# Kernel optimization log

Measured on AMD Instinct MI355X. Metric: run time of the kernel, lower is better.

Reference implementation:

```python
import jax, jax.numpy as jnp
import numpy as np

N = 100000        # nodes
E = 1_600_000     # edges (avg degree 16)
IN = 128          # in_feats
HID = 64          # hidden_feats
H = 3             # num_heads
OUT = 16          # out_feats
NEG_SLOPE = 0.2   # DGL GATConv default LeakyReLU slope


def setup_inputs() -> dict:
    key = jax.random.key(0)
    ks = jax.random.split(key, 16)
    f = lambda k, shape, s=0.1: (jax.random.normal(k, shape, jnp.float32) * s)
    return {
        "features": f(ks[0], (N, IN), 1.0),
        "src": jax.random.randint(ks[1], (E,), 0, N),
        "dst": jax.random.randint(ks[2], (E,), 0, N),
        # GATConv 1: in -> (H, HID)
        "W1": f(ks[3], (IN, H * HID)),
        "al1": f(ks[4], (H, HID)),
        "ar1": f(ks[5], (H, HID)),
        "b1": f(ks[6], (H, HID)),
        # GATConv 2: H*HID -> (H, HID)
        "W2": f(ks[7], (H * HID, H * HID)),
        "al2": f(ks[8], (H, HID)),
        "ar2": f(ks[9], (H, HID)),
        "b2": f(ks[10], (H, HID)),
        # MLP head
        "w3": f(ks[11], (H * HID, HID)),
        "b3": f(ks[12], (HID,)),
        "w4": f(ks[13], (HID, OUT)),
        "b4": f(ks[14], (OUT,)),
    }


def gat_layer(x, src, dst, W, al, ar, b):
    # feat: (N, H, D) projected features
    feat = (x @ W).reshape(-1, H, HID)
    el = jnp.einsum('nhd,hd->nh', feat, al)   # (N, H)
    er = jnp.einsum('nhd,hd->nh', feat, ar)   # (N, H)
    e = el[src] + er[dst]                     # (E, H) edge scores
    e = jnp.where(e > 0, e, NEG_SLOPE * e)    # LeakyReLU
    # numerically stable softmax over incoming edges of each dst node
    m = jax.lax.stop_gradient(jax.ops.segment_max(e, dst, num_segments=N))
    ex = jnp.exp(e - m[dst])
    s = jax.ops.segment_sum(ex, dst, num_segments=N)
    alpha = ex / s[dst]                       # (E, H)
    # message passing: scatter alpha-weighted src features to dst
    out = jax.ops.segment_sum(alpha[:, :, None] * feat[src], dst, num_segments=N)
    return jax.nn.relu(out + b)               # (N, H, D)


def reference(features, src, dst, W1, al1, ar1, b1, W2, al2, ar2, b2, w3, b3, w4, b4):
    x = gat_layer(features, src, dst, W1, al1, ar1, b1).reshape(N, H * HID)
    x = gat_layer(x, src, dst, W2, al2, ar2, b2).reshape(N, H * HID)
    h = jax.nn.relu(x @ w3 + b3)
    return h @ w4 + b4
```

## Files before the change

kernel.cpp:

```cpp
#include <hip/hip_runtime.h>
#include <cstdint>
#include <cstddef>

#define NN   100000
#define EE   1600000
#define INF_ 128
#define HIDF 64
#define NH   3
#define FEAT 192
#define OUTF 16
#define NEG  0.2f

#define NI4  25000
#define NB   98

typedef unsigned short ushort_t;
typedef unsigned int   uint_t;

__device__ __forceinline__ float bf2f(ushort_t u) {
    return __uint_as_float(((uint_t)u) << 16);
}
__device__ __forceinline__ ushort_t f2bf(float f) {
    uint_t b = __float_as_uint(f);
    return (ushort_t)((b + 0x7FFFu + ((b >> 16) & 1u)) >> 16);
}


__global__ void hist_kernel(const int* __restrict__ dst, int* __restrict__ counts) {
    int e = blockIdx.x * 256 + threadIdx.x;
    if (e < EE) atomicAdd(&counts[dst[e]], 1);
}

__global__ __launch_bounds__(256) void blocksum_kernel(const int* __restrict__ counts,
                                                       int* __restrict__ bsum) {
    int t = threadIdx.x;
    int idx4 = blockIdx.x * 256 + t;
    int s = 0;
    if (idx4 < NI4) {
        int4 v = ((const int4*)counts)[idx4];
        s = v.x + v.y + v.z + v.w;
    }
    __shared__ int sd[4];
    for (int o = 32; o; o >>= 1) s += __shfl_down(s, o, 64);
    if ((t & 63) == 0) sd[t >> 6] = s;
    __syncthreads();
    if (t == 0) bsum[blockIdx.x] = sd[0] + sd[1] + sd[2] + sd[3];
}

__global__ __launch_bounds__(128) void scanb_kernel(int* __restrict__ bsum) {
    __shared__ int sd[128];
    int t = threadIdx.x;
    int v = (t < NB) ? bsum[t] : 0;
    sd[t] = v;
    __syncthreads();
    for (int o = 1; o < 128; o <<= 1) {
        int u = (t >= o) ? sd[t - o] : 0;
        __syncthreads();
        sd[t] += u;
        __syncthreads();
    }
    if (t < NB) bsum[t] = sd[t] - v;
}

__global__ __launch_bounds__(256) void scanfinal_kernel(const int* __restrict__ counts,
                                                        const int* __restrict__ bsum,
                                                        int* __restrict__ row_ptr,
                                                        int* __restrict__ cursor) {
    __shared__ int sd[256];
    int t = threadIdx.x;
    int idx4 = blockIdx.x * 256 + t;
    int4 v = make_int4(0, 0, 0, 0);
    if (idx4 < NI4) v = ((const int4*)counts)[idx4];
    int s = v.x + v.y + v.z + v.w;
    sd[t] = s;
    __syncthreads();
    for (int o = 1; o < 256; o <<= 1) {
        int u = (t >= o) ? sd[t - o] : 0;
        __syncthreads();
        sd[t] += u;
        __syncthreads();
    }
    int base = bsum[blockIdx.x] + sd[t] - s;
    if (idx4 < NI4) {
        int4 r;
        r.x = base;
        r.y = base + v.x;
        r.z = base + v.x + v.y;
        r.w = base + v.x + v.y + v.z;
        ((int4*)row_ptr)[idx4] = r;
        ((int4*)cursor)[idx4]  = r;
    }
    if (blockIdx.x == 0 && t == 0) row_ptr[NN] = EE;
}

__global__ void scatter_kernel(const int* __restrict__ src, const int* __restrict__ dst,
                               int* __restrict__ cursor, int* __restrict__ ssrc,
                               int* __restrict__ sdst) {
    int e = blockIdx.x * 256 + threadIdx.x;
    if (e < EE) {
        int d = dst[e];
        int p = atomicAdd(&cursor[d], 1);
        ssrc[p] = src[e];
        sdst[p] = d;
    }
}


__global__ __launch_bounds__(256) void edgew_kernel(const int* __restrict__ ssrc,
                                                    const int* __restrict__ sdst,
                                                    const float* __restrict__ el,
                                                    const float* __restrict__ er,
                                                    float* __restrict__ wgt) {
    int p = blockIdx.x * 256 + threadIdx.x;
    if (p >= EE) return;
    int s = ssrc[p], d = sdst[p];
    float a0 = el[s * 3 + 0] + er[d * 3 + 0]; a0 = a0 > 0.f ? a0 : NEG * a0;
    float a1 = el[s * 3 + 1] + er[d * 3 + 1]; a1 = a1 > 0.f ? a1 : NEG * a1;
    float a2 = el[s * 3 + 2] + er[d * 3 + 2]; a2 = a2 > 0.f ? a2 : NEG * a2;
    wgt[p * 3 + 0] = __expf(a0);
    wgt[p * 3 + 1] = __expf(a1);
    wgt[p * 3 + 2] = __expf(a2);
}


template <int K, int N, bool BIAS, bool RELU, bool ELER, bool A_BF16, bool C_BF16>
__global__ __launch_bounds__(256) void gemm64_kernel(const void* __restrict__ Av,
                                                     const float* __restrict__ B,
                                                     const float* __restrict__ bias,
                                                     void* __restrict__ Cv,
                                                     const float* __restrict__ al,
                                                     const float* __restrict__ ar,
                                                     float* __restrict__ el,
                                                     float* __restrict__ er) {
    __shared__ float As[32][64];
    __shared__ float Bs[32][64];
    const int m0 = blockIdx.x * 64;
    const int n0 = blockIdx.y * 64;
    const int t  = threadIdx.x;
    const int tr = t >> 4;
    const int tc = t & 15;

    float acc[4][4] = {};

    for (int kt = 0; kt < K; kt += 32) {
        if (A_BF16) {
            const ushort_t* A = (const ushort_t*)Av;
            int row = t >> 2, c8 = (t & 3) * 8;
            int gr = m0 + row;
            if (gr < NN) {
                uint4 v = *(const uint4*)(A + (size_t)gr * K + kt + c8);
                As[c8 + 0][row] = bf2f((ushort_t)(v.x & 0xffff));
                As[c8 + 1][row] = bf2f((ushort_t)(v.x >> 16));
                As[c8 + 2][row] = bf2f((ushort_t)(v.y & 0xffff));
                As[c8 + 3][row] = bf2f((ushort_t)(v.y >> 16));
                As[c8 + 4][row] = bf2f((ushort_t)(v.z & 0xffff));
                As[c8 + 5][row] = bf2f((ushort_t)(v.z >> 16));
                As[c8 + 6][row] = bf2f((ushort_t)(v.w & 0xffff));
                As[c8 + 7][row] = bf2f((ushort_t)(v.w >> 16));
            } else {
#pragma unroll
                for (int j = 0; j < 8; ++j) As[c8 + j][row] = 0.f;
            }
        } else {
            const float* A = (const float*)Av;
            int f = t;
#pragma unroll
            for (int it = 0; it < 2; ++it, f += 256) {
                int row = f >> 3, c4 = (f & 7) * 4;
                float4 v = make_float4(0.f, 0.f, 0.f, 0.f);
                int gr = m0 + row;
                if (gr < NN) v = *(const float4*)(A + (size_t)gr * K + kt + c4);
                As[c4 + 0][row] = v.x;
                As[c4 + 1][row] = v.y;
                As[c4 + 2][row] = v.z;
                As[c4 + 3][row] = v.w;
            }
        }
        {
            int f = t;
#pragma unroll
            for (int it = 0; it < 2; ++it, f += 256) {
                int row = f >> 4, c4 = (f & 15) * 4;
                *(float4*)&Bs[row][c4] = *(const float4*)(B + (size_t)(kt + row) * N + n0 + c4);
            }
        }
        __syncthreads();
#pragma unroll
        for (int k = 0; k < 32; ++k) {
            float4 a = *(const float4*)&As[k][tr * 4];
            float4 b = *(const float4*)&Bs[k][tc * 4];
            acc[0][0] += a.x * b.x; acc[0][1] += a.x * b.y; acc[0][2] += a.x * b.z; acc[0][3] += a.x * b.w;
            acc[1][0] += a.y * b.x; acc[1][1] += a.y * b.y; acc[1][2] += a.y * b.z; acc[1][3] += a.y * b.w;
            acc[2][0] += a.z * b.x; acc[2][1] += a.z * b.y; acc[2][2] += a.z * b.z; acc[2][3] += a.z * b.w;
            acc[3][0] += a.w * b.x; acc[3][1] += a.w * b.y; acc[3][2] += a.w * b.z; acc[3][3] += a.w * b.w;
        }
        __syncthreads();
    }

    float4 bv = make_float4(0.f, 0.f, 0.f, 0.f);
    if (BIAS) bv = *(const float4*)(bias + n0 + tc * 4);
#pragma unroll
    for (int i = 0; i < 4; ++i) {
        int row = m0 + tr * 4 + i;
        if (row >= NN) continue;
        float4 r;
        r.x = acc[i][0]; r.y = acc[i][1]; r.z = acc[i][2]; r.w = acc[i][3];
        if (BIAS) { r.x += bv.x; r.y += bv.y; r.z += bv.z; r.w += bv.w; }
        if (RELU) {
            r.x = fmaxf(r.x, 0.f); r.y = fmaxf(r.y, 0.f);
            r.z = fmaxf(r.z, 0.f); r.w = fmaxf(r.w, 0.f);
        }
        if (C_BF16) {
            ushort4 u;
            u.x = f2bf(r.x); u.y = f2bf(r.y); u.z = f2bf(r.z); u.w = f2bf(r.w);
            *(ushort4*)((ushort_t*)Cv + (size_t)row * N + n0 + tc * 4) = u;
        } else {
            *(float4*)((float*)Cv + (size_t)row * N + n0 + tc * 4) = r;
        }
    }

    if (ELER) {
        const int h = blockIdx.y;
        float4 va = *(const float4*)(al + h * HIDF + tc * 4);
        float4 vb = *(const float4*)(ar + h * HIDF + tc * 4);
#pragma unroll
        for (int i = 0; i < 4; ++i) {
            float pl = acc[i][0] * va.x + acc[i][1] * va.y + acc[i][2] * va.z + acc[i][3] * va.w;
            float pr = acc[i][0] * vb.x + acc[i][1] * vb.y + acc[i][2] * vb.z + acc[i][3] * vb.w;
#pragma unroll
            for (int o = 1; o < 16; o <<= 1) {
                pl += __shfl_xor(pl, o, 16);
                pr += __shfl_xor(pr, o, 16);
            }
            int row = m0 + tr * 4 + i;
            if (tc == 0 && row < NN) {
                el[row * NH + h] = pl;
                er[row * NH + h] = pr;
            }
        }
    }
}


template <int K, int M, int ROWS, bool BIAS, bool RELU>
__global__ void rowgemm_kernel(const float* __restrict__ A, const float* __restrict__ W,
                               const float* __restrict__ bias, float* __restrict__ C) {
    __shared__ float a[ROWS][K];
    const int BT = M * ROWS;
    int r0 = blockIdx.x * ROWS;
    for (int i = threadIdx.x; i < ROWS * K; i += BT) {
        int rr = i / K, kk = i - rr * K;
        int row = r0 + rr;
        a[rr][kk] = (row < NN) ? A[(size_t)row * K + kk] : 0.f;
    }
    __syncthreads();
    int rr = threadIdx.x / M, c = threadIdx.x - rr * M;
    int row = r0 + rr;
    if (row >= NN) return;
    float acc = 0.f;
#pragma unroll
    for (int k = 0; k < K; ++k) acc += a[rr][k] * W[k * M + c];
    if (BIAS) acc += bias[c];
    if (RELU) acc = fmaxf(acc, 0.f);
    C[(size_t)row * M + c] = acc;
}


__global__ __launch_bounds__(256) void aggregate_kernel(
    const int* __restrict__ row_ptr, const int* __restrict__ ssrc,
    const float* __restrict__ wgt,
    const ushort_t* __restrict__ featb, const float* __restrict__ bias,
    ushort_t* __restrict__ outb) {
    int w = blockIdx.x * 4 + (threadIdx.x >> 6);
    if (w >= NN) return;
    int lane = threadIdx.x & 63;
    int beg = row_ptr[w], end = row_ptr[w + 1];

    float s0 = 0.f, s1 = 0.f, s2 = 0.f;
    float acc0 = 0.f, acc1 = 0.f, acc2 = 0.f;
    for (int p = beg; p < end; ++p) {
        int s = __builtin_amdgcn_readfirstlane(ssrc[p]);
        float w0 = wgt[p * 3 + 0];
        float w1 = wgt[p * 3 + 1];
        float w2 = wgt[p * 3 + 2];
        s0 += w0; s1 += w1; s2 += w2;
        const ushort_t* fr = featb + (size_t)s * FEAT;
        acc0 += w0 * bf2f(fr[lane]);
        acc1 += w1 * bf2f(fr[64 + lane]);
        acc2 += w2 * bf2f(fr[128 + lane]);
    }

    float r0, r1, r2;
    if (end > beg) { r0 = acc0 / s0; r1 = acc1 / s1; r2 = acc2 / s2; }
    else           { r0 = r1 = r2 = 0.f; }
    r0 += bias[lane]; r1 += bias[64 + lane]; r2 += bias[128 + lane];
    outb[(size_t)w * FEAT + lane]       = f2bf(fmaxf(r0, 0.f));
    outb[(size_t)w * FEAT + 64 + lane]  = f2bf(fmaxf(r1, 0.f));
    outb[(size_t)w * FEAT + 128 + lane] = f2bf(fmaxf(r2, 0.f));
}


extern "C" void kernel_launch(void* const* d_in, const int* in_sizes, int n_in,
                              void* d_out, int out_size, void* d_ws, size_t ws_size,
                              hipStream_t stream) {
    const float* features = (const float*)d_in[0];
    const int*   src      = (const int*)d_in[1];
    const int*   dst      = (const int*)d_in[2];
    const float* W1  = (const float*)d_in[3];
    const float* al1 = (const float*)d_in[4];
    const float* ar1 = (const float*)d_in[5];
    const float* b1  = (const float*)d_in[6];
    const float* W2  = (const float*)d_in[7];
    const float* al2 = (const float*)d_in[8];
    const float* ar2 = (const float*)d_in[9];
    const float* b2  = (const float*)d_in[10];
    const float* w3  = (const float*)d_in[11];
    const float* b3  = (const float*)d_in[12];
    const float* w4  = (const float*)d_in[13];
    const float* b4  = (const float*)d_in[14];
    float* out = (float*)d_out;

    char* p = (char*)d_ws;
    ushort_t* featb = (ushort_t*)p; p += (size_t)NN * FEAT * 2;
    ushort_t* xb    = (ushort_t*)p; p += (size_t)NN * FEAT * 2;
    float* scratch  = (float*)p;    p += (size_t)NN * HIDF * 4;
    float* el  = (float*)p; p += (size_t)NN * NH * 4;
    float* er  = (float*)p; p += (size_t)NN * NH * 4;
    int* counts  = (int*)p;  p += (size_t)NN * 4;
    int* row_ptr = (int*)p;  p += (size_t)(NN + 4) * 4;
    int* cursor  = (int*)p;  p += (size_t)NN * 4;
    int* ssrc    = (int*)p;  p += (size_t)EE * 4;
    int* sdst    = (int*)p;  p += (size_t)EE * 4;
    int* bsum    = (int*)p;  p += 128 * 4;

    float* wgt = scratch;
    float* hid = scratch;

    const int GM = (NN + 63) / 64;
    const int GE = (EE + 255) / 256;

    hipMemsetAsync(counts, 0, (size_t)NN * 4, stream);
    hist_kernel<<<GE, 256, 0, stream>>>(dst, counts);
    blocksum_kernel<<<NB, 256, 0, stream>>>(counts, bsum);
    scanb_kernel<<<1, 128, 0, stream>>>(bsum);
    scanfinal_kernel<<<NB, 256, 0, stream>>>(counts, bsum, row_ptr, cursor);
    scatter_kernel<<<GE, 256, 0, stream>>>(src, dst, cursor, ssrc, sdst);

    gemm64_kernel<INF_, FEAT, false, false, true, false, true>
        <<<dim3(GM, FEAT / 64), 256, 0, stream>>>(features, W1, nullptr, featb, al1, ar1, el, er);
    edgew_kernel<<<GE, 256, 0, stream>>>(ssrc, sdst, el, er, wgt);
    aggregate_kernel<<<(NN + 3) / 4, 256, 0, stream>>>(row_ptr, ssrc, wgt, featb, b1, xb);

    gemm64_kernel<FEAT, FEAT, false, false, true, true, true>
        <<<dim3(GM, FEAT / 64), 256, 0, stream>>>(xb, W2, nullptr, featb, al2, ar2, el, er);
    edgew_kernel<<<GE, 256, 0, stream>>>(ssrc, sdst, el, er, wgt);
    aggregate_kernel<<<(NN + 3) / 4, 256, 0, stream>>>(row_ptr, ssrc, wgt, featb, b2, xb);

    gemm64_kernel<FEAT, HIDF, true, true, false, true, false>
        <<<dim3(GM, 1), 256, 0, stream>>>(xb, w3, b3, hid, nullptr, nullptr, nullptr, nullptr);
    rowgemm_kernel<HIDF, OUTF, 16, true, false><<<NN / 16, 256, 0, stream>>>(hid, w4, b4, out);
}
```

Before: 889.5 us.

## Load edge indices and weights cooperatively per wavefront and broadcast via shuffles

Edge softmax weights are stored as three separate per-head arrays instead of interleaved triples. The aggregation kernel now loads up to 64 edge source indices and weights at once with coalesced per-lane loads. It reduces the denominators with a butterfly shuffle and broadcasts each edge's index and weights via shuffles in the inner loop. This replaces serialized per-edge uniform loads, whose latency sits on the critical path of the gather, at the cost of extra shuffle instructions per edge.

```diff
diff --git a/kernel.cpp b/kernel.cpp
--- a/kernel.cpp
+++ b/kernel.cpp
@@ -110,16 +110,18 @@
                                                     const int* __restrict__ sdst,
                                                     const float* __restrict__ el,
                                                     const float* __restrict__ er,
-                                                    float* __restrict__ wgt) {
+                                                    float* __restrict__ wgt0,
+                                                    float* __restrict__ wgt1,
+                                                    float* __restrict__ wgt2) {
     int p = blockIdx.x * 256 + threadIdx.x;
     if (p >= EE) return;
     int s = ssrc[p], d = sdst[p];
     float a0 = el[s * 3 + 0] + er[d * 3 + 0]; a0 = a0 > 0.f ? a0 : NEG * a0;
     float a1 = el[s * 3 + 1] + er[d * 3 + 1]; a1 = a1 > 0.f ? a1 : NEG * a1;
     float a2 = el[s * 3 + 2] + er[d * 3 + 2]; a2 = a2 > 0.f ? a2 : NEG * a2;
-    wgt[p * 3 + 0] = __expf(a0);
-    wgt[p * 3 + 1] = __expf(a1);
-    wgt[p * 3 + 2] = __expf(a2);
+    wgt0[p] = __expf(a0);
+    wgt1[p] = __expf(a1);
+    wgt2[p] = __expf(a2);
 }
 
 
@@ -268,7 +270,8 @@
 
 __global__ __launch_bounds__(256) void aggregate_kernel(
     const int* __restrict__ row_ptr, const int* __restrict__ ssrc,
-    const float* __restrict__ wgt,
+    const float* __restrict__ wgt0, const float* __restrict__ wgt1,
+    const float* __restrict__ wgt2,
     const ushort_t* __restrict__ featb, const float* __restrict__ bias,
     ushort_t* __restrict__ outb) {
     int w = blockIdx.x * 4 + (threadIdx.x >> 6);
@@ -278,16 +281,36 @@
 
     float s0 = 0.f, s1 = 0.f, s2 = 0.f;
     float acc0 = 0.f, acc1 = 0.f, acc2 = 0.f;
-    for (int p = beg; p < end; ++p) {
-        int s = __builtin_amdgcn_readfirstlane(ssrc[p]);
-        float w0 = wgt[p * 3 + 0];
-        float w1 = wgt[p * 3 + 1];
-        float w2 = wgt[p * 3 + 2];
-        s0 += w0; s1 += w1; s2 += w2;
-        const ushort_t* fr = featb + (size_t)s * FEAT;
-        acc0 += w0 * bf2f(fr[lane]);
-        acc1 += w1 * bf2f(fr[64 + lane]);
-        acc2 += w2 * bf2f(fr[128 + lane]);
+
+    for (int c = beg; c < end; c += 64) {
+        int n = min(64, end - c);
+        int   sv  = 0;
+        float wv0 = 0.f, wv1 = 0.f, wv2 = 0.f;
+        if (lane < n) {
+            sv  = ssrc[c + lane];
+            wv0 = wgt0[c + lane];
+            wv1 = wgt1[c + lane];
+            wv2 = wgt2[c + lane];
+        }
+        float t0 = wv0, t1 = wv1, t2 = wv2;
+#pragma unroll
+        for (int o = 1; o < 64; o <<= 1) {
+            t0 += __shfl_xor(t0, o, 64);
+            t1 += __shfl_xor(t1, o, 64);
+            t2 += __shfl_xor(t2, o, 64);
+        }
+        s0 += t0; s1 += t1; s2 += t2;
+
+        for (int i = 0; i < n; ++i) {
+            int   s  = __shfl(sv, i, 64);
+            float w0 = __shfl(wv0, i, 64);
+            float w1 = __shfl(wv1, i, 64);
+            float w2 = __shfl(wv2, i, 64);
+            const ushort_t* fr = featb + (size_t)s * FEAT;
+            acc0 += w0 * bf2f(fr[lane]);
+            acc1 += w1 * bf2f(fr[64 + lane]);
+            acc2 += w2 * bf2f(fr[128 + lane]);
+        }
     }
 
     float r0, r1, r2;
@@ -333,8 +356,10 @@
     int* sdst    = (int*)p;  p += (size_t)EE * 4;
     int* bsum    = (int*)p;  p += 128 * 4;
 
-    float* wgt = scratch;
-    float* hid = scratch;
+    float* wgt0 = scratch;
+    float* wgt1 = scratch + EE;
+    float* wgt2 = scratch + 2 * (size_t)EE;
+    float* hid  = scratch;
 
     const int GM = (NN + 63) / 64;
     const int GE = (EE + 255) / 256;
@@ -348,13 +373,13 @@
 
     gemm64_kernel<INF_, FEAT, false, false, true, false, true>
         <<<dim3(GM, FEAT / 64), 256, 0, stream>>>(features, W1, nullptr, featb, al1, ar1, el, er);
-    edgew_kernel<<<GE, 256, 0, stream>>>(ssrc, sdst, el, er, wgt);
-    aggregate_kernel<<<(NN + 3) / 4, 256, 0, stream>>>(row_ptr, ssrc, wgt, featb, b1, xb);
+    edgew_kernel<<<GE, 256, 0, stream>>>(ssrc, sdst, el, er, wgt0, wgt1, wgt2);
+    aggregate_kernel<<<(NN + 3) / 4, 256, 0, stream>>>(row_ptr, ssrc, wgt0, wgt1, wgt2, featb, b1, xb);
 
     gemm64_kernel<FEAT, FEAT, false, false, true, true, true>
         <<<dim3(GM, FEAT / 64), 256, 0, stream>>>(xb, W2, nullptr, featb, al2, ar2, el, er);
-    edgew_kernel<<<GE, 256, 0, stream>>>(ssrc, sdst, el, er, wgt);
-    aggregate_kernel<<<(NN + 3) / 4, 256, 0, stream>>>(row_ptr, ssrc, wgt, featb, b2, xb);
+    edgew_kernel<<<GE, 256, 0, stream>>>(ssrc, sdst, el, er, wgt0, wgt1, wgt2);
+    aggregate_kernel<<<(NN + 3) / 4, 256, 0, stream>>>(row_ptr, ssrc, wgt0, wgt1, wgt2, featb, b2, xb);
 
     gemm64_kernel<FEAT, HIDF, true, true, false, true, false>
         <<<dim3(GM, 1), 256, 0, stream>>>(xb, w3, b3, hid, nullptr, nullptr, nullptr, nullptr);
```

Result: faster. 779.0 us (-12.4%).
